# Performance work log

Measured on AMD Instinct MI355X. Metric: run time of the kernel, lower is better.

The kernel has to match this reference:

```python
import jax, jax.numpy as jnp
import numpy as np

DIM = 1024
NUM_HEADS = 16
HEAD_DIM = DIM // NUM_HEADS
GATE_HID = DIM // 4


def setup_inputs() -> dict:
    key = jax.random.key(0)
    ks = jax.random.split(key, 16)
    B, S, D = 2, 2048, DIM
    sc = 1.0 / np.sqrt(D)
    inp = {
        "h": jax.random.normal(ks[0], (B, S, D), jnp.float32),
        "x": jax.random.normal(ks[1], (B, S, D), jnp.float32),
        # attention projections, stored (in, out) so y = x @ W + b
        "Wq": jax.random.normal(ks[2], (D, D), jnp.float32) * sc,
        "bq": jnp.zeros((D,), jnp.float32),
        "Wk": jax.random.normal(ks[3], (D, D), jnp.float32) * sc,
        "bk": jnp.zeros((D,), jnp.float32),
        "Wv": jax.random.normal(ks[4], (D, D), jnp.float32) * sc,
        "bv": jnp.zeros((D,), jnp.float32),
        "Wo": jax.random.normal(ks[5], (D, D), jnp.float32) * sc,
        "bo": jnp.zeros((D,), jnp.float32),
        # gating MLP: Linear(2D -> D//4) -> GELU -> Linear(D//4 -> D) -> sigmoid
        "Wg1": jax.random.normal(ks[6], (2 * D, GATE_HID), jnp.float32) * (1.0 / np.sqrt(2 * D)),
        "bg1": jnp.zeros((GATE_HID,), jnp.float32),
        "Wg2": jax.random.normal(ks[7], (GATE_HID, D), jnp.float32) * (1.0 / np.sqrt(GATE_HID)),
        "bg2": jnp.zeros((D,), jnp.float32),
    }
    return inp


def reference(h, x, Wq, bq, Wk, bk, Wv, bv, Wo, bo, Wg1, bg1, Wg2, bg2):
    B, S, D = h.shape
    # gated blend of latent h and input x
    gate_in = jnp.concatenate([h, x], axis=-1)                      # (B,S,2D)
    gate = jax.nn.sigmoid((jax.nn.gelu(gate_in @ Wg1 + bg1, approximate=False)) @ Wg2 + bg2)
    blended = gate * h + (1.0 - gate) * x                           # (B,S,D)
    # multi-head self-attention
    q = (blended @ Wq + bq).reshape(B, S, NUM_HEADS, HEAD_DIM)
    k = (blended @ Wk + bk).reshape(B, S, NUM_HEADS, HEAD_DIM)
    v = (blended @ Wv + bv).reshape(B, S, NUM_HEADS, HEAD_DIM)
    scale = 1.0 / np.sqrt(HEAD_DIM).astype(np.float32)
    scores = jnp.einsum('bqhd,bkhd->bhqk', q, k) * scale            # (B,H,S,S)
    attn = jax.nn.softmax(scores, axis=-1)
    out = jnp.einsum('bhqk,bkhd->bqhd', attn, v).reshape(B, S, D)
    return out @ Wo + bo
```

## Files before the change

### kernel.cpp

```cpp
#include <hip/hip_runtime.h>
#include <hip/hip_bf16.h>


typedef __attribute__((ext_vector_type(4))) unsigned int u32x4;
typedef __attribute__((ext_vector_type(2))) unsigned int u32x2;
typedef __attribute__((ext_vector_type(8))) short s16x8;
typedef __attribute__((ext_vector_type(8))) unsigned short u16x8;
typedef __attribute__((ext_vector_type(4))) unsigned short u16x4;
typedef __attribute__((ext_vector_type(4))) float f32x4;

#define QSCALE 0.18033688011112043f
#define FIXED_M 24.0f

__device__ __forceinline__ unsigned short f2bf(float f) {
    unsigned int i = __builtin_bit_cast(unsigned int, f) + 0x8000u;
    return (unsigned short)(i >> 16);
}
__device__ __forceinline__ unsigned int pack2bf(float a, float b) {
    unsigned int ia = __builtin_bit_cast(unsigned int, a) + 0x8000u;
    unsigned int ib = __builtin_bit_cast(unsigned int, b) + 0x8000u;
    return __builtin_amdgcn_perm(ib, ia, 0x07060302u);
}

__device__ __forceinline__ void gload16(const void* g, void* l) {
    __builtin_amdgcn_global_load_lds(
        (const __attribute__((address_space(1))) void*)g,
        (__attribute__((address_space(3))) void*)l, 16, 0, 0);
}

struct TEntry { const float* src; unsigned short* dst; int K; int N; };
struct TTable { TEntry e[6]; };

__global__ __launch_bounds__(256) void prep_all(
    TTable tt,
    const float* __restrict__ bq, const float* __restrict__ bk,
    const float* __restrict__ bv, float* __restrict__ bqkv)
{
    const int bid = (int)blockIdx.x;
    const int tid = threadIdx.x;
    if (bid < 3072) {
        const TEntry E = tt.e[bid >> 9];
        const int bx = bid & 511;
        const int ntn = E.N >> 5;
        if (bx >= (E.K >> 6) * ntn) return;
        const int n0 = (bx % ntn) * 32, k0 = (bx / ntn) * 64;
        __shared__ float tile[64][33];
        const int lnn = tid & 31, lkk = tid >> 5;
#pragma unroll
        for (int i = 0; i < 8; ++i)
            tile[lkk + i * 8][lnn] = E.src[(size_t)(k0 + lkk + i * 8) * E.N + n0 + lnn];
        __syncthreads();
        const int snn = tid >> 3, skk = (tid & 7) * 8;
        u16x8 o;
#pragma unroll
        for (int j = 0; j < 8; ++j) o[j] = f2bf(tile[skk + j][snn]);
        *reinterpret_cast<u16x8*>(&E.dst[(size_t)(n0 + snn) * E.K + k0 + skk]) = o;
        return;
    }
    const int i = (bid - 3072) * 256 + tid;
    if (i < 1024) bqkv[i] = bq[i];
    else if (i < 2048) bqkv[i] = bk[i - 1024];
    else if (i < 3072) bqkv[i] = bv[i - 2048];
}

__global__ __launch_bounds__(256) void transpose_v(
    const unsigned short* __restrict__ qkv, unsigned short* __restrict__ vt)
{
    __shared__ unsigned short t[64][65];
    const int st = blockIdx.x;
    const int bh = blockIdx.y;
    const int b = bh >> 4, h = bh & 15;
    const int tx = threadIdx.x & 63, ty = threadIdx.x >> 6;
    const int s0 = st * 64;
    const size_t base = (size_t)(b * 2048 + s0) * 3072 + 2048 + h * 64;
#pragma unroll
    for (int i = 0; i < 16; ++i)
        t[ty + i * 4][tx] = qkv[base + (size_t)(ty + i * 4) * 3072 + tx];
    __syncthreads();
    const size_t obase = (size_t)(bh * 64) * 2048 + s0;
#pragma unroll
    for (int i = 0; i < 16; ++i)
        vt[obase + (size_t)(ty + i * 4) * 2048 + tx] = t[tx][ty + i * 4];
}

enum { EPI_GELU = 1, EPI_BLEND = 2, EPI_F32 = 3, EPI_QKV = 4 };

template <int EPI>
__global__ __launch_bounds__(256, 3) void gemm_kernel(
    const unsigned short* __restrict__ A, int lda,
    const unsigned short* __restrict__ Bt, int ldb,
    const float* __restrict__ bias,
    void* __restrict__ Cv, int ldc, int K,
    const float* __restrict__ hb, const float* __restrict__ xb,
    int swzn, int ntn)
{
    __shared__ unsigned short Alds[2][128 * 32];
    __shared__ unsigned short Blds[2][128 * 32];

    const int tid = threadIdx.x;
    const int lane = tid & 63;
    const int w = tid >> 6;
    const int wr = w >> 1, wc = w & 1;
    int mt, nt;
    if (swzn > 0) {
        const int xcd = (int)blockIdx.x & 7, seq = (int)blockIdx.x >> 3;
        nt = xcd * swzn + seq % swzn;
        mt = seq / swzn;
    } else {
        nt = (int)blockIdx.x % ntn;
        mt = (int)blockIdx.x / ntn;
    }
    const int m0 = mt * 128, n0 = nt * 128;
    const int lrow = lane & 15, lko = (lane >> 4) * 8;

    const int grow = w * 32 + (lane >> 2);
    const int gk8 = (lane & 3) * 8;
    const unsigned short* ga0 = A + (size_t)(m0 + grow) * lda + gk8;
    const unsigned short* ga1 = ga0 + (size_t)16 * lda;
    const unsigned short* gb0 = Bt + (size_t)(n0 + grow) * ldb + gk8;
    const unsigned short* gb1 = gb0 + (size_t)16 * ldb;

    auto stage = [&](int buf, int k0) {
        unsigned short* la = &Alds[buf][w * 1024];
        unsigned short* lb = &Blds[buf][w * 1024];
        gload16(ga0 + k0, la);
        gload16(ga1 + k0, la + 512);
        gload16(gb0 + k0, lb);
        gload16(gb1 + k0, lb + 512);
    };

    f32x4 acc[4][4];
#pragma unroll
    for (int i = 0; i < 4; ++i)
#pragma unroll
        for (int j = 0; j < 4; ++j) acc[i][j] = (f32x4){0.f, 0.f, 0.f, 0.f};

    const int kks = K >> 5;
    stage(0, 0);
    __syncthreads();

    for (int t = 0; t < kks; ++t) {
        const int cur = t & 1;
        if (t + 1 < kks) stage(cur ^ 1, (t + 1) << 5);

        s16x8 af[4], bfr[4];
#pragma unroll
        for (int mi = 0; mi < 4; ++mi)
            af[mi] = *reinterpret_cast<const s16x8*>(&Alds[cur][(wr * 64 + mi * 16 + lrow) * 32 + lko]);
#pragma unroll
        for (int ni = 0; ni < 4; ++ni)
            bfr[ni] = *reinterpret_cast<const s16x8*>(&Blds[cur][(wc * 64 + ni * 16 + lrow) * 32 + lko]);
#pragma unroll
        for (int mi = 0; mi < 4; ++mi)
#pragma unroll
            for (int ni = 0; ni < 4; ++ni)
                acc[mi][ni] = __builtin_amdgcn_mfma_f32_16x16x32_bf16(af[mi], bfr[ni], acc[mi][ni], 0, 0, 0);

        __syncthreads();
    }

    const int rbase = m0 + wr * 64;
    const int cbase = n0 + wc * 64;
#pragma unroll
    for (int mi = 0; mi < 4; ++mi) {
#pragma unroll
        for (int j = 0; j < 4; ++j) {
            const int r = rbase + mi * 16 + (lane >> 4) * 4 + j;
#pragma unroll
            for (int ni = 0; ni < 4; ++ni) {
                const int c = cbase + ni * 16 + (lane & 15);
                float v = acc[mi][ni][j] + bias[c];
                if constexpr (EPI == EPI_GELU) {
                    float g = 0.5f * v * (1.f + erff(v * 0.70710678118654752f));
                    ((unsigned short*)Cv)[(size_t)r * ldc + c] = f2bf(g);
                } else if constexpr (EPI == EPI_BLEND) {
                    float gate = 1.f / (1.f + __expf(-v));
                    const size_t o = (size_t)r * ldc + c;
                    float bl = gate * hb[o] + (1.f - gate) * xb[o];
                    ((unsigned short*)Cv)[o] = f2bf(bl);
                } else if constexpr (EPI == EPI_QKV) {
                    const float scl = (c < 1024) ? QSCALE : 1.f;
                    ((unsigned short*)Cv)[(size_t)r * ldc + c] = f2bf(v * scl);
                } else {
                    ((float*)Cv)[(size_t)r * ldc + c] = v;
                }
            }
        }
    }
}

template <int EPI>
__global__ __launch_bounds__(256, 4) void gemm64_kernel(
    const unsigned short* __restrict__ A, int lda,
    const unsigned short* __restrict__ Bt, int ldb,
    const float* __restrict__ bias,
    void* __restrict__ Cv, int ldc, int K,
    const float* __restrict__ hb, const float* __restrict__ xb,
    int swzn)
{
    __shared__ unsigned short Alds[2][64 * 32];
    __shared__ unsigned short Blds[2][64 * 32];

    const int tid = threadIdx.x;
    const int lane = tid & 63;
    const int w = tid >> 6;
    const int wr = w >> 1, wc = w & 1;
    const int xcd = (int)blockIdx.x & 7, seq = (int)blockIdx.x >> 3;
    const int nt = xcd * swzn + seq % swzn;
    const int mt = seq / swzn;
    const int m0 = mt * 64, n0 = nt * 64;
    const int lrow = lane & 15, lko = (lane >> 4) * 8;

    const int grow = w * 16 + (lane >> 2);
    const int gk8 = (lane & 3) * 8;
    const unsigned short* ga = A + (size_t)(m0 + grow) * lda + gk8;
    const unsigned short* gb = Bt + (size_t)(n0 + grow) * ldb + gk8;

    auto stage = [&](int buf, int k0) {
        gload16(ga + k0, &Alds[buf][w * 512]);
        gload16(gb + k0, &Blds[buf][w * 512]);
    };

    f32x4 acc[2][2];
#pragma unroll
    for (int i = 0; i < 2; ++i)
#pragma unroll
        for (int j = 0; j < 2; ++j) acc[i][j] = (f32x4){0.f, 0.f, 0.f, 0.f};

    const int kks = K >> 5;
    stage(0, 0);
    __syncthreads();

    for (int t = 0; t < kks; ++t) {
        const int cur = t & 1;
        if (t + 1 < kks) stage(cur ^ 1, (t + 1) << 5);

        s16x8 af[2], bfr[2];
#pragma unroll
        for (int mi = 0; mi < 2; ++mi)
            af[mi] = *reinterpret_cast<const s16x8*>(&Alds[cur][(wr * 32 + mi * 16 + lrow) * 32 + lko]);
#pragma unroll
        for (int ni = 0; ni < 2; ++ni)
            bfr[ni] = *reinterpret_cast<const s16x8*>(&Blds[cur][(wc * 32 + ni * 16 + lrow) * 32 + lko]);
#pragma unroll
        for (int mi = 0; mi < 2; ++mi)
#pragma unroll
            for (int ni = 0; ni < 2; ++ni)
                acc[mi][ni] = __builtin_amdgcn_mfma_f32_16x16x32_bf16(af[mi], bfr[ni], acc[mi][ni], 0, 0, 0);

        __syncthreads();
    }

    const int rbase = m0 + wr * 32;
    const int cbase = n0 + wc * 32;
#pragma unroll
    for (int mi = 0; mi < 2; ++mi) {
#pragma unroll
        for (int j = 0; j < 4; ++j) {
            const int r = rbase + mi * 16 + (lane >> 4) * 4 + j;
#pragma unroll
            for (int ni = 0; ni < 2; ++ni) {
                const int c = cbase + ni * 16 + (lane & 15);
                float v = acc[mi][ni][j] + bias[c];
                if constexpr (EPI == EPI_BLEND) {
                    float gate = 1.f / (1.f + __expf(-v));
                    const size_t o = (size_t)r * ldc + c;
                    float bl = gate * hb[o] + (1.f - gate) * xb[o];
                    ((unsigned short*)Cv)[o] = f2bf(bl);
                } else {
                    ((float*)Cv)[(size_t)r * ldc + c] = v;
                }
            }
        }
    }
}

__global__ __launch_bounds__(256, 4) void gelu_partial(
    const float* __restrict__ h, const float* __restrict__ x,
    const unsigned short* __restrict__ Bt,
    float* __restrict__ partial)
{
    __shared__ unsigned short Alds[2][32 * 32];
    __shared__ unsigned short Blds[2][256 * 32];

    const int tid = threadIdx.x;
    const int lane = tid & 63;
    const int w = tid >> 6;
    const int mt = (int)blockIdx.x >> 2, ks = (int)blockIdx.x & 3;
    const int m0 = mt * 32, kbase = ks * 512;
    const int lrow = lane & 15, lko = (lane >> 4) * 8;

    const int arl = tid >> 3, ac4 = (tid & 7) * 4;
    const size_t arg = (size_t)(m0 + arl) * 1024;
    auto loadA = [&](int k0, f32x4& v) {
        v = *reinterpret_cast<const f32x4*>((k0 < 1024 ? h : x) + arg + (k0 & 1023) + ac4);
    };
    auto writeA = [&](int buf, const f32x4& v) {
        u32x2 p = {pack2bf(v[0], v[1]), pack2bf(v[2], v[3])};
        *reinterpret_cast<u32x2*>(&Alds[buf][arl * 32 + ac4]) = p;
    };

    const int brow = w * 64 + (lane >> 2);
    const int bk8 = (lane & 3) * 8;
    const unsigned short* gb = Bt + (size_t)brow * 2048 + kbase + bk8;
    auto stageB = [&](int buf, int k0) {
#pragma unroll
        for (int i = 0; i < 4; ++i)
            gload16(gb + (size_t)(i * 16) * 2048 + k0, &Blds[buf][(w * 64 + i * 16) * 32]);
    };

    f32x4 acc[2][4];
#pragma unroll
    for (int i = 0; i < 2; ++i)
#pragma unroll
        for (int j = 0; j < 4; ++j) acc[i][j] = (f32x4){0.f, 0.f, 0.f, 0.f};

    f32x4 areg;
    loadA(kbase, areg);
    stageB(0, 0);
    writeA(0, areg);
    __syncthreads();

    for (int t = 0; t < 16; ++t) {
        const int cur = t & 1;
        if (t + 1 < 16) {
            loadA(kbase + ((t + 1) << 5), areg);
            stageB(cur ^ 1, (t + 1) << 5);
        }

        s16x8 af[2], bfr[4];
#pragma unroll
        for (int mi = 0; mi < 2; ++mi)
            af[mi] = *reinterpret_cast<const s16x8*>(&Alds[cur][(mi * 16 + lrow) * 32 + lko]);
#pragma unroll
        for (int ni = 0; ni < 4; ++ni)
            bfr[ni] = *reinterpret_cast<const s16x8*>(&Blds[cur][(w * 64 + ni * 16 + lrow) * 32 + lko]);
#pragma unroll
        for (int mi = 0; mi < 2; ++mi)
#pragma unroll
            for (int ni = 0; ni < 4; ++ni)
                acc[mi][ni] = __builtin_amdgcn_mfma_f32_16x16x32_bf16(af[mi], bfr[ni], acc[mi][ni], 0, 0, 0);

        if (t + 1 < 16) writeA(cur ^ 1, areg);
        __syncthreads();
    }

    float* pbase = partial + (size_t)ks * 4096 * 256;
#pragma unroll
    for (int mi = 0; mi < 2; ++mi) {
#pragma unroll
        for (int j = 0; j < 4; ++j) {
            const int r = m0 + mi * 16 + (lane >> 4) * 4 + j;
#pragma unroll
            for (int ni = 0; ni < 4; ++ni) {
                const int c = w * 64 + ni * 16 + (lane & 15);
                pbase[(size_t)r * 256 + c] = acc[mi][ni][j];
            }
        }
    }
}

__global__ __launch_bounds__(256) void gelu_reduce(
    const float* __restrict__ partial, const float* __restrict__ bias,
    unsigned short* __restrict__ g1)
{
    const size_t idx = ((size_t)blockIdx.x * 256 + threadIdx.x) * 4;
    const int c = (int)(idx & 255);
    f32x4 s = *reinterpret_cast<const f32x4*>(partial + idx);
#pragma unroll
    for (int ks = 1; ks < 4; ++ks) {
        f32x4 p = *reinterpret_cast<const f32x4*>(partial + (size_t)ks * 4096 * 256 + idx);
        s[0] += p[0]; s[1] += p[1]; s[2] += p[2]; s[3] += p[3];
    }
    f32x4 bb = *reinterpret_cast<const f32x4*>(bias + c);
    u16x4 o;
#pragma unroll
    for (int j = 0; j < 4; ++j) {
        float v = s[j] + bb[j];
        o[j] = f2bf(0.5f * v * (1.f + erff(v * 0.70710678118654752f)));
    }
    *reinterpret_cast<u16x4*>(g1 + idx) = o;
}

#define ALD 72

__global__ __launch_bounds__(256, 3) void attn_kernel(
    const unsigned short* __restrict__ qkv,
    const unsigned short* __restrict__ vt,
    unsigned short* __restrict__ out)
{
    __shared__ unsigned short Klds[2][64 * 64];
    __shared__ unsigned short Vlds[2][64 * 64];
    __shared__ unsigned short Plds[4][16 * ALD];

    const int tid = threadIdx.x, lane = tid & 63, w = tid >> 6;
    const int xcd = (int)blockIdx.x & 7, seq = (int)blockIdx.x >> 3;
    const int bh = xcd * 4 + (seq & 3);
    const int qt = seq >> 2;
    const int b = bh >> 4, h = bh & 15;
    const int rb = b * 2048;
    const int lrow = lane & 15, g = lane >> 4, lko = g * 8;

    s16x8 qf[2][2];
#pragma unroll
    for (int qg = 0; qg < 2; ++qg) {
        const size_t qrow = (size_t)(rb + qt * 128 + w * 32 + qg * 16 + lrow) * 3072 + h * 64;
        qf[qg][0] = *reinterpret_cast<const s16x8*>(qkv + qrow + lko);
        qf[qg][1] = *reinterpret_cast<const s16x8*>(qkv + qrow + 32 + lko);
    }

    const int grow = w * 16 + (lane >> 3);
    const int gswz = ((lane & 7) ^ (lane >> 3)) * 8;
    const unsigned short* kgp = qkv + (size_t)(rb + grow) * 3072 + 1024 + h * 64 + gswz;
    const unsigned short* vgp = vt + (size_t)(bh * 64 + grow) * 2048 + gswz;

    auto stage = [&](int buf, int t0) {
        gload16(kgp + (size_t)t0 * 3072, &Klds[buf][w * 1024]);
        gload16(kgp + (size_t)(t0 + 8) * 3072, &Klds[buf][w * 1024 + 512]);
        gload16(vgp + t0, &Vlds[buf][w * 1024]);
        gload16(vgp + t0 + 8 * 2048, &Vlds[buf][w * 1024 + 512]);
    };

    const int cs0 = ((g) ^ (lrow & 7)) * 8;
    const int cs1 = ((4 + g) ^ (lrow & 7)) * 8;

    f32x4 acc0[4], acc1[4];
#pragma unroll
    for (int di = 0; di < 4; ++di) {
        acc0[di] = (f32x4){0.f, 0.f, 0.f, 0.f};
        acc1[di] = (f32x4){0.f, 0.f, 0.f, 0.f};
    }
    float lsum0 = 0.f, lsum1 = 0.f;

    unsigned short* pw = &Plds[w][0];
    s16x8 vf[2][4];

    stage(0, 0);
    __syncthreads();

    for (int t0 = 0; t0 < 2048; t0 += 64) {
        const int cur = (t0 >> 6) & 1;
        if (t0 + 64 < 2048) stage(cur ^ 1, t0 + 64);

        if (t0 > 0) {
#pragma unroll
            for (int st = 0; st < 2; ++st) {
                s16x8 pf = *reinterpret_cast<const s16x8*>(&pw[lrow * ALD + st * 32 + lko]);
#pragma unroll
                for (int di = 0; di < 4; ++di)
                    acc1[di] = __builtin_amdgcn_mfma_f32_16x16x32_bf16(vf[st][di], pf, acc1[di], 0, 0, 0);
            }
        }

        s16x8 kf[4][2];
#pragma unroll
        for (int ni = 0; ni < 4; ++ni) {
            kf[ni][0] = *reinterpret_cast<const s16x8*>(&Klds[cur][(ni * 16 + lrow) * 64 + cs0]);
            kf[ni][1] = *reinterpret_cast<const s16x8*>(&Klds[cur][(ni * 16 + lrow) * 64 + cs1]);
        }

        f32x4 s0[4];
#pragma unroll
        for (int ni = 0; ni < 4; ++ni) s0[ni] = (f32x4){0.f, 0.f, 0.f, 0.f};
#pragma unroll
        for (int ni = 0; ni < 4; ++ni)
#pragma unroll
            for (int fi = 0; fi < 2; ++fi)
                s0[ni] = __builtin_amdgcn_mfma_f32_16x16x32_bf16(kf[ni][fi], qf[0][fi], s0[ni], 0, 0, 0);

#pragma unroll
        for (int ni = 0; ni < 4; ++ni) {
            float p0 = __builtin_amdgcn_exp2f(s0[ni][0] - FIXED_M);
            float p1 = __builtin_amdgcn_exp2f(s0[ni][1] - FIXED_M);
            float p2 = __builtin_amdgcn_exp2f(s0[ni][2] - FIXED_M);
            float p3 = __builtin_amdgcn_exp2f(s0[ni][3] - FIXED_M);
            lsum0 += (p0 + p1) + (p2 + p3);
            u32x2 pk = {pack2bf(p0, p1), pack2bf(p2, p3)};
            *reinterpret_cast<u32x2*>(&pw[lrow * ALD + ni * 16 + g * 4]) = pk;
        }

        f32x4 s1[4];
#pragma unroll
        for (int ni = 0; ni < 4; ++ni) s1[ni] = (f32x4){0.f, 0.f, 0.f, 0.f};
#pragma unroll
        for (int ni = 0; ni < 4; ++ni)
#pragma unroll
            for (int fi = 0; fi < 2; ++fi)
                s1[ni] = __builtin_amdgcn_mfma_f32_16x16x32_bf16(kf[ni][fi], qf[1][fi], s1[ni], 0, 0, 0);

#pragma unroll
        for (int di = 0; di < 4; ++di) {
            vf[0][di] = *reinterpret_cast<const s16x8*>(&Vlds[cur][(di * 16 + lrow) * 64 + cs0]);
            vf[1][di] = *reinterpret_cast<const s16x8*>(&Vlds[cur][(di * 16 + lrow) * 64 + cs1]);
        }

#pragma unroll
        for (int st = 0; st < 2; ++st) {
            s16x8 pf = *reinterpret_cast<const s16x8*>(&pw[lrow * ALD + st * 32 + lko]);
#pragma unroll
            for (int di = 0; di < 4; ++di)
                acc0[di] = __builtin_amdgcn_mfma_f32_16x16x32_bf16(vf[st][di], pf, acc0[di], 0, 0, 0);
        }

#pragma unroll
        for (int ni = 0; ni < 4; ++ni) {
            float p0 = __builtin_amdgcn_exp2f(s1[ni][0] - FIXED_M);
            float p1 = __builtin_amdgcn_exp2f(s1[ni][1] - FIXED_M);
            float p2 = __builtin_amdgcn_exp2f(s1[ni][2] - FIXED_M);
            float p3 = __builtin_amdgcn_exp2f(s1[ni][3] - FIXED_M);
            lsum1 += (p0 + p1) + (p2 + p3);
            u32x2 pk = {pack2bf(p0, p1), pack2bf(p2, p3)};
            *reinterpret_cast<u32x2*>(&pw[lrow * ALD + ni * 16 + g * 4]) = pk;
        }

        __syncthreads();
    }

#pragma unroll
    for (int st = 0; st < 2; ++st) {
        s16x8 pf = *reinterpret_cast<const s16x8*>(&pw[lrow * ALD + st * 32 + lko]);
#pragma unroll
        for (int di = 0; di < 4; ++di)
            acc1[di] = __builtin_amdgcn_mfma_f32_16x16x32_bf16(vf[st][di], pf, acc1[di], 0, 0, 0);
    }

    lsum0 += __shfl_xor(lsum0, 16);
    lsum0 += __shfl_xor(lsum0, 32);
    lsum1 += __shfl_xor(lsum1, 16);
    lsum1 += __shfl_xor(lsum1, 32);
    const float inv0 = 1.f / lsum0;
    const float inv1 = 1.f / lsum1;
    const size_t orow0 = (size_t)(rb + qt * 128 + w * 32 + lrow) * 1024 + h * 64;
    const size_t orow1 = orow0 + (size_t)16 * 1024;
#pragma unroll
    for (int di = 0; di < 4; ++di) {
        u32x2 ov0 = {pack2bf(acc0[di][0] * inv0, acc0[di][1] * inv0),
                     pack2bf(acc0[di][2] * inv0, acc0[di][3] * inv0)};
        *reinterpret_cast<u32x2*>(&out[orow0 + di * 16 + g * 4]) = ov0;
        u32x2 ov1 = {pack2bf(acc1[di][0] * inv1, acc1[di][1] * inv1),
                     pack2bf(acc1[di][2] * inv1, acc1[di][3] * inv1)};
        *reinterpret_cast<u32x2*>(&out[orow1 + di * 16 + g * 4]) = ov1;
    }
}

extern "C" void kernel_launch(void* const* d_in, const int* in_sizes, int n_in,
                              void* d_out, int out_size, void* d_ws, size_t ws_size,
                              hipStream_t stream)
{
    const float* h   = (const float*)d_in[0];
    const float* x   = (const float*)d_in[1];
    const float* Wq  = (const float*)d_in[2];
    const float* bq  = (const float*)d_in[3];
    const float* Wk  = (const float*)d_in[4];
    const float* bk  = (const float*)d_in[5];
    const float* Wv  = (const float*)d_in[6];
    const float* bv  = (const float*)d_in[7];
    const float* Wo  = (const float*)d_in[8];
    const float* bo  = (const float*)d_in[9];
    const float* Wg1 = (const float*)d_in[10];
    const float* bg1 = (const float*)d_in[11];
    const float* Wg2 = (const float*)d_in[12];
    const float* bg2 = (const float*)d_in[13];

    char* ws = (char*)d_ws;
    size_t off = 0;
    auto alloc = [&](size_t bytes) {
        void* p = ws + off;
        off += (bytes + 255) & ~(size_t)255;
        return p;
    };
    unsigned short* wg1T  = (unsigned short*)alloc((size_t)256 * 2048 * 2);
    unsigned short* wg2T  = (unsigned short*)alloc((size_t)1024 * 256 * 2);
    unsigned short* wqkvT = (unsigned short*)alloc((size_t)3072 * 1024 * 2);
    unsigned short* woT   = (unsigned short*)alloc((size_t)1024 * 1024 * 2);
    float*          bqkv  = (float*)alloc((size_t)3072 * 4);
    unsigned short* blend = (unsigned short*)alloc((size_t)4096 * 1024 * 2);
    unsigned short* attno = (unsigned short*)alloc((size_t)4096 * 1024 * 2);
    unsigned short* vtb   = (unsigned short*)alloc((size_t)32 * 64 * 2048 * 2);
    unsigned short* g1    = (unsigned short*)alloc((size_t)4096 * 256 * 2);
    unsigned short* qkv   = (unsigned short*)alloc((size_t)4096 * 3072 * 2);
    float* partial = (float*)qkv;
    (void)ws_size; (void)in_sizes; (void)n_in; (void)out_size;

    TTable tt;
    tt.e[0] = {Wg1, wg1T, 2048, 256};
    tt.e[1] = {Wg2, wg2T, 256, 1024};
    tt.e[2] = {Wq, wqkvT, 1024, 1024};
    tt.e[3] = {Wk, wqkvT + (size_t)1024 * 1024, 1024, 1024};
    tt.e[4] = {Wv, wqkvT + (size_t)2048 * 1024, 1024, 1024};
    tt.e[5] = {Wo, woT, 1024, 1024};
    prep_all<<<3072 + 12, 256, 0, stream>>>(tt, bq, bk, bv, bqkv);

    gelu_partial<<<512, 256, 0, stream>>>(h, x, wg1T, partial);
    gelu_reduce<<<1024, 256, 0, stream>>>(partial, bg1, g1);
    gemm64_kernel<EPI_BLEND><<<1024, 256, 0, stream>>>(
        g1, 256, wg2T, 256, bg2, blend, 1024, 256, h, x, 2);

    gemm_kernel<EPI_QKV><<<768, 256, 0, stream>>>(
        blend, 1024, wqkvT, 1024, bqkv, qkv, 3072, 1024, nullptr, nullptr, 3, 24);

    transpose_v<<<dim3(32, 32), 256, 0, stream>>>(qkv, vtb);

    attn_kernel<<<512, 256, 0, stream>>>(qkv, vtb, attno);

    gemm64_kernel<EPI_F32><<<1024, 256, 0, stream>>>(
        attno, 1024, woT, 1024, bo, (float*)d_out, 1024, 1024, nullptr, nullptr, 2);
}
```

Baseline: 148.8 us.

## Double-buffer P tiles, defer both PV MFMAs, fold max offset into accumulator init

Gives each wave a second P buffer so both query sub-tiles' probabilities persist. Both PV products are then deferred to the next iteration, leaving the QK MFMAs and exp work uninterrupted within an iteration. It also seeds the score accumulators with -FIXED_M so the per-element subtraction before exp2 disappears, and raises wave priority around MFMA blocks with s_setprio. The cost is extra LDS per block, which may reduce occupancy, plus more live vf registers across iterations.

```diff
diff --git a/kernel.cpp b/kernel.cpp
--- a/kernel.cpp
+++ b/kernel.cpp
@@ -391,7 +391,7 @@
 {
     __shared__ unsigned short Klds[2][64 * 64];
     __shared__ unsigned short Vlds[2][64 * 64];
-    __shared__ unsigned short Plds[4][16 * ALD];
+    __shared__ unsigned short Plds[2][4][16 * ALD];
 
     const int tid = threadIdx.x, lane = tid & 63, w = tid >> 6;
     const int xcd = (int)blockIdx.x & 7, seq = (int)blockIdx.x >> 3;
@@ -432,7 +432,8 @@
     }
     float lsum0 = 0.f, lsum1 = 0.f;
 
-    unsigned short* pw = &Plds[w][0];
+    unsigned short* pw0 = &Plds[0][w][0];
+    unsigned short* pw1 = &Plds[1][w][0];
     s16x8 vf[2][4];
 
     stage(0, 0);
@@ -443,13 +444,22 @@
         if (t0 + 64 < 2048) stage(cur ^ 1, t0 + 64);
 
         if (t0 > 0) {
+            __builtin_amdgcn_s_setprio(1);
 #pragma unroll
             for (int st = 0; st < 2; ++st) {
-                s16x8 pf = *reinterpret_cast<const s16x8*>(&pw[lrow * ALD + st * 32 + lko]);
+                s16x8 pf0 = *reinterpret_cast<const s16x8*>(&pw0[lrow * ALD + st * 32 + lko]);
 #pragma unroll
                 for (int di = 0; di < 4; ++di)
-                    acc1[di] = __builtin_amdgcn_mfma_f32_16x16x32_bf16(vf[st][di], pf, acc1[di], 0, 0, 0);
+                    acc0[di] = __builtin_amdgcn_mfma_f32_16x16x32_bf16(vf[st][di], pf0, acc0[di], 0, 0, 0);
             }
+#pragma unroll
+            for (int st = 0; st < 2; ++st) {
+                s16x8 pf1 = *reinterpret_cast<const s16x8*>(&pw1[lrow * ALD + st * 32 + lko]);
+#pragma unroll
+                for (int di = 0; di < 4; ++di)
+                    acc1[di] = __builtin_amdgcn_mfma_f32_16x16x32_bf16(vf[st][di], pf1, acc1[di], 0, 0, 0);
+            }
+            __builtin_amdgcn_s_setprio(0);
         }
 
         s16x8 kf[4][2];
@@ -461,32 +471,38 @@
 
         f32x4 s0[4];
 #pragma unroll
-        for (int ni = 0; ni < 4; ++ni) s0[ni] = (f32x4){0.f, 0.f, 0.f, 0.f};
+        for (int ni = 0; ni < 4; ++ni)
+            s0[ni] = (f32x4){-FIXED_M, -FIXED_M, -FIXED_M, -FIXED_M};
+        __builtin_amdgcn_s_setprio(1);
 #pragma unroll
         for (int ni = 0; ni < 4; ++ni)
 #pragma unroll
             for (int fi = 0; fi < 2; ++fi)
                 s0[ni] = __builtin_amdgcn_mfma_f32_16x16x32_bf16(kf[ni][fi], qf[0][fi], s0[ni], 0, 0, 0);
+        __builtin_amdgcn_s_setprio(0);
 
 #pragma unroll
         for (int ni = 0; ni < 4; ++ni) {
-            float p0 = __builtin_amdgcn_exp2f(s0[ni][0] - FIXED_M);
-            float p1 = __builtin_amdgcn_exp2f(s0[ni][1] - FIXED_M);
-            float p2 = __builtin_amdgcn_exp2f(s0[ni][2] - FIXED_M);
-            float p3 = __builtin_amdgcn_exp2f(s0[ni][3] - FIXED_M);
+            float p0 = __builtin_amdgcn_exp2f(s0[ni][0]);
+            float p1 = __builtin_amdgcn_exp2f(s0[ni][1]);
+            float p2 = __builtin_amdgcn_exp2f(s0[ni][2]);
+            float p3 = __builtin_amdgcn_exp2f(s0[ni][3]);
             lsum0 += (p0 + p1) + (p2 + p3);
             u32x2 pk = {pack2bf(p0, p1), pack2bf(p2, p3)};
-            *reinterpret_cast<u32x2*>(&pw[lrow * ALD + ni * 16 + g * 4]) = pk;
+            *reinterpret_cast<u32x2*>(&pw0[lrow * ALD + ni * 16 + g * 4]) = pk;
         }
 
         f32x4 s1[4];
 #pragma unroll
-        for (int ni = 0; ni < 4; ++ni) s1[ni] = (f32x4){0.f, 0.f, 0.f, 0.f};
+        for (int ni = 0; ni < 4; ++ni)
+            s1[ni] = (f32x4){-FIXED_M, -FIXED_M, -FIXED_M, -FIXED_M};
+        __builtin_amdgcn_s_setprio(1);
 #pragma unroll
         for (int ni = 0; ni < 4; ++ni)
 #pragma unroll
             for (int fi = 0; fi < 2; ++fi)
                 s1[ni] = __builtin_amdgcn_mfma_f32_16x16x32_bf16(kf[ni][fi], qf[1][fi], s1[ni], 0, 0, 0);
+        __builtin_amdgcn_s_setprio(0);
 
 #pragma unroll
         for (int di = 0; di < 4; ++di) {
@@ -495,22 +511,14 @@
         }
 
 #pragma unroll
-        for (int st = 0; st < 2; ++st) {
-            s16x8 pf = *reinterpret_cast<const s16x8*>(&pw[lrow * ALD + st * 32 + lko]);
-#pragma unroll
-            for (int di = 0; di < 4; ++di)
-                acc0[di] = __builtin_amdgcn_mfma_f32_16x16x32_bf16(vf[st][di], pf, acc0[di], 0, 0, 0);
-        }
-
-#pragma unroll
         for (int ni = 0; ni < 4; ++ni) {
-            float p0 = __builtin_amdgcn_exp2f(s1[ni][0] - FIXED_M);
-            float p1 = __builtin_amdgcn_exp2f(s1[ni][1] - FIXED_M);
-            float p2 = __builtin_amdgcn_exp2f(s1[ni][2] - FIXED_M);
-            float p3 = __builtin_amdgcn_exp2f(s1[ni][3] - FIXED_M);
+            float p0 = __builtin_amdgcn_exp2f(s1[ni][0]);
+            float p1 = __builtin_amdgcn_exp2f(s1[ni][1]);
+            float p2 = __builtin_amdgcn_exp2f(s1[ni][2]);
+            float p3 = __builtin_amdgcn_exp2f(s1[ni][3]);
             lsum1 += (p0 + p1) + (p2 + p3);
             u32x2 pk = {pack2bf(p0, p1), pack2bf(p2, p3)};
-            *reinterpret_cast<u32x2*>(&pw[lrow * ALD + ni * 16 + g * 4]) = pk;
+            *reinterpret_cast<u32x2*>(&pw1[lrow * ALD + ni * 16 + g * 4]) = pk;
         }
 
         __syncthreads();
@@ -518,10 +526,17 @@
 
 #pragma unroll
     for (int st = 0; st < 2; ++st) {
-        s16x8 pf = *reinterpret_cast<const s16x8*>(&pw[lrow * ALD + st * 32 + lko]);
+        s16x8 pf0 = *reinterpret_cast<const s16x8*>(&pw0[lrow * ALD + st * 32 + lko]);
 #pragma unroll
         for (int di = 0; di < 4; ++di)
-            acc1[di] = __builtin_amdgcn_mfma_f32_16x16x32_bf16(vf[st][di], pf, acc1[di], 0, 0, 0);
+            acc0[di] = __builtin_amdgcn_mfma_f32_16x16x32_bf16(vf[st][di], pf0, acc0[di], 0, 0, 0);
+    }
+#pragma unroll
+    for (int st = 0; st < 2; ++st) {
+        s16x8 pf1 = *reinterpret_cast<const s16x8*>(&pw1[lrow * ALD + st * 32 + lko]);
+#pragma unroll
+        for (int di = 0; di < 4; ++di)
+            acc1[di] = __builtin_amdgcn_mfma_f32_16x16x32_bf16(vf[st][di], pf1, acc1[di], 0, 0, 0);
     }
 
     lsum0 += __shfl_xor(lsum0, 16);
```

Measured after the change: 147.8 us, median of 3. About the same (-0.7%).
